# Kernel optimization log

Hardware: AMD Instinct MI355X
Metric: run time of the kernel (lower is better)

## Reference

```python
import jax, jax.numpy as jnp
import numpy as np

N_HEADS = 16
NEG_BIAS = -1000000000.0


def setup_inputs() -> dict:
    key = jax.random.key(0)
    k1, k2, k3, k4 = jax.random.split(key, 4)
    B, S, D = 2, 2048, 1024
    queries = jax.random.normal(k1, (B, S, D), dtype=jnp.float32)
    keys = jax.random.normal(k2, (B, S, D), dtype=jnp.float32)
    values = jax.random.normal(k3, (B, S, D), dtype=jnp.float32)
    mask = jax.random.randint(k4, (B, S, S), 0, 2, dtype=jnp.int32)
    return {"queries": queries, "keys": keys, "values": values, "mask": mask}


def _split_heads(x):
    B, S, D = x.shape
    return x.reshape(B, S, N_HEADS, D // N_HEADS).transpose(0, 2, 1, 3)  # [B,H,S,d]


def reference(queries, keys, values, mask):
    q = _split_heads(queries)   # [B,H,Sq,d]
    k = _split_heads(keys)      # [B,H,Sk,d]
    v = _split_heads(values)    # [B,H,Sk,d]
    d_head = q.shape[-1]
    # scaled dot product similarity
    sim = jnp.einsum('bhqd,bhkd->bhqk', q, k) / jnp.sqrt(jnp.float32(d_head))
    # additive mask (softmax attention function -> non-hadamard)
    bias = NEG_BIAS * (1.0 - mask.astype(sim.dtype))[:, None]  # [B,1,Sq,Sk]
    sim = sim + bias
    # softmax with max-subtraction (numerically stable, as in original)
    weights = jax.nn.softmax(sim, axis=-1)
    out = jnp.einsum('bhqk,bhkd->bhqd', weights, v)  # [B,H,Sq,d]
    B, H, Sq, d = out.shape
    return out.transpose(0, 2, 1, 3).reshape(B, Sq, H * d)
```

## Files before the change

### kernel.cpp

```cpp
#include <hip/hip_runtime.h>

#define S_LEN 2048
#define D_MODEL 1024
#define DH 64
#define BQ 64
#define BK 64
#define LDK 72
#define LDV 72
#define LDP 72
#define ZSCALE 0.18033688f
#define M0F    12.0f
#define ZBIAS  -1.5e9f

using short8 = __attribute__((ext_vector_type(8))) short;
using f32x4  = __attribute__((ext_vector_type(4))) float;
using uint2v = __attribute__((ext_vector_type(2))) unsigned int;

__device__ __forceinline__ unsigned short f2bf(float x) {
    union { float f; unsigned int u; } c; c.f = x;
    unsigned int u = c.u;
    u += 0x7fffu + ((u >> 16) & 1u);
    return (unsigned short)(u >> 16);
}

__global__ __launch_bounds__(256) void cvt_fused(const float* __restrict__ V,
                                                 const int* __restrict__ M,
                                                 const float* __restrict__ K,
                                                 unsigned short* __restrict__ VT,
                                                 unsigned long long* __restrict__ Mb,
                                                 unsigned short* __restrict__ KB) {
    const int blk = blockIdx.x;
    const int tid = threadIdx.x;
    if (blk < 1024) {
        __shared__ float tsF[64][65];
        const int b  = blk >> 9;
        const int h  = (blk >> 5) & 15;
        const int s0 = (blk & 31) * 64;
        #pragma unroll
        for (int it = 0; it < 2; ++it) {
            int seg = tid + it * 256;
            int s = seg >> 3, d8 = (seg & 7) << 3;
            const float* p = V + (size_t)(b * S_LEN + s0 + s) * D_MODEL + h * DH + d8;
            f32x4 a = *(const f32x4*)p;
            f32x4 c = *(const f32x4*)(p + 4);
            #pragma unroll
            for (int j = 0; j < 4; ++j) { tsF[s][d8 + j] = a[j]; tsF[s][d8 + 4 + j] = c[j]; }
        }
        __syncthreads();
        #pragma unroll
        for (int it = 0; it < 2; ++it) {
            int seg = tid + it * 256;
            int d = seg >> 3, s8 = (seg & 7) << 3;
            short8 w;
            #pragma unroll
            for (int j = 0; j < 8; ++j) w[j] = (short)f2bf(tsF[s8 + j][d]);
            *(short8*)(VT + ((size_t)((b * 16 + h) * 64 + d)) * S_LEN + s0 + s8) = w;
        }
    } else if (blk < 2048) {
        const int pb   = blk - 1024;
        const int wave = tid >> 6, lane = tid & 63;
        const int row  = pb * 4 + wave;
        const int* mp  = M + (size_t)row * S_LEN;
        #pragma unroll 4
        for (int it = 0; it < 32; ++it) {
            int m = mp[it * 64 + lane];
            unsigned long long bal = __ballot(m != 0);
            if (lane == 0) Mb[(size_t)row * 32 + it] = bal;
        }
    } else {
        size_t g = (size_t)(blk - 2048) * 256 + tid;
        size_t base = g * 16;
        f32x4 a0 = *(const f32x4*)(K + base);
        f32x4 a1 = *(const f32x4*)(K + base + 4);
        f32x4 a2 = *(const f32x4*)(K + base + 8);
        f32x4 a3 = *(const f32x4*)(K + base + 12);
        short8 w0, w1;
        #pragma unroll
        for (int j = 0; j < 4; ++j) {
            w0[j] = (short)f2bf(a0[j]); w0[4 + j] = (short)f2bf(a1[j]);
            w1[j] = (short)f2bf(a2[j]); w1[4 + j] = (short)f2bf(a3[j]);
        }
        *(short8*)(KB + base)     = w0;
        *(short8*)(KB + base + 8) = w1;
    }
}

__global__ __launch_bounds__(256) void mha_fwd_v3(
    const float* __restrict__ Q,
    const float* __restrict__ K,
    const unsigned short* __restrict__ KB,
    const unsigned short* __restrict__ VT,
    const unsigned int* __restrict__ Mw,
    float* __restrict__ O,
    int kbf)
{
    __shared__ alignas(16) unsigned short Ks[BK][LDK];
    __shared__ alignas(16) unsigned short Vt[DH][LDV];
    __shared__ alignas(16) unsigned short Ps[4][16][LDP];

    const int blk = blockIdx.x;
    const int b   = blk >> 9;
    const int h   = (blk >> 5) & 15;
    const int qbase = (blk & 31) * BQ;
    const int bh  = b * 16 + h;

    const int tid  = threadIdx.x;
    const int wave = tid >> 6;
    const int lane = tid & 63;
    const int n16  = lane & 15;
    const int quad = lane >> 4;

    const size_t qoff = (size_t)(b * S_LEN + qbase + wave * 16 + n16) * D_MODEL + h * DH + quad * 8;
    short8 qf0, qf1;
    {
        f32x4 a0 = *(const f32x4*)(Q + qoff);
        f32x4 a1 = *(const f32x4*)(Q + qoff + 4);
        f32x4 a2 = *(const f32x4*)(Q + qoff + 32);
        f32x4 a3 = *(const f32x4*)(Q + qoff + 36);
        #pragma unroll
        for (int j = 0; j < 4; ++j) {
            qf0[j] = (short)f2bf(a0[j]); qf0[4 + j] = (short)f2bf(a1[j]);
            qf1[j] = (short)f2bf(a2[j]); qf1[4 + j] = (short)f2bf(a3[j]);
        }
    }

    const short8 ones = {0x3F80,0x3F80,0x3F80,0x3F80,0x3F80,0x3F80,0x3F80,0x3F80};

    f32x4 o0 = {0.f,0.f,0.f,0.f}, o1 = o0, o2 = o0, o3 = o0, o4 = o0;

    size_t mwbase[4];
    #pragma unroll
    for (int r = 0; r < 4; ++r)
        mwbase[r] = ((size_t)(b * S_LEN + qbase + wave * 16 + quad * 4 + r)) * 64;

    for (int kb = 0; kb < S_LEN; kb += BK) {
        __syncthreads();
        if (kbf) {
            int seg = tid;
            #pragma unroll
            for (int it = 0; it < 2; ++it, seg += 256) {
                int row = seg >> 3, c8 = (seg & 7) << 3;
                *(short8*)&Ks[row][c8] =
                    *(const short8*)(KB + (size_t)(b * S_LEN + kb + row) * D_MODEL + h * DH + c8);
            }
        } else {
            int seg = tid;
            #pragma unroll
            for (int it = 0; it < 2; ++it, seg += 256) {
                int row = seg >> 3, c8 = (seg & 7) << 3;
                const float* kp = K + (size_t)(b * S_LEN + kb + row) * D_MODEL + h * DH + c8;
                f32x4 p0 = *(const f32x4*)kp;
                f32x4 p1 = *(const f32x4*)(kp + 4);
                short8 w;
                #pragma unroll
                for (int j = 0; j < 4; ++j) { w[j] = (short)f2bf(p0[j]); w[4 + j] = (short)f2bf(p1[j]); }
                *(short8*)&Ks[row][c8] = w;
            }
        }
        {
            int seg = tid;
            #pragma unroll
            for (int it = 0; it < 2; ++it, seg += 256) {
                int d = seg >> 3, k8 = (seg & 7) << 3;
                *(short8*)&Vt[d][k8] =
                    *(const short8*)(VT + ((size_t)(bh * 64 + d)) * S_LEN + kb + k8);
            }
        }
        __syncthreads();

        f32x4 s[4];
        #pragma unroll
        for (int ct = 0; ct < 4; ++ct) {
            short8 kf0 = *(const short8*)&Ks[ct * 16 + n16][     quad * 8];
            short8 kf1 = *(const short8*)&Ks[ct * 16 + n16][32 + quad * 8];
            f32x4 acc = {0.f,0.f,0.f,0.f};
            acc = __builtin_amdgcn_mfma_f32_16x16x32_bf16(qf0, kf0, acc, 0, 0, 0);
            acc = __builtin_amdgcn_mfma_f32_16x16x32_bf16(qf1, kf1, acc, 0, 0, 0);
            s[ct] = acc;
        }
        #pragma unroll
        for (int r = 0; r < 4; ++r) {
            uint2v mv = *(const uint2v*)(Mw + mwbase[r] + (kb >> 5));
            unsigned int b0 = mv[0] >> n16, b1 = mv[1] >> n16;
            s[0][r] = fmaf(s[0][r], ZSCALE, (b0 & 1u)         ? -M0F : ZBIAS);
            s[1][r] = fmaf(s[1][r], ZSCALE, ((b0 >> 16) & 1u) ? -M0F : ZBIAS);
            s[2][r] = fmaf(s[2][r], ZSCALE, (b1 & 1u)         ? -M0F : ZBIAS);
            s[3][r] = fmaf(s[3][r], ZSCALE, ((b1 >> 16) & 1u) ? -M0F : ZBIAS);
        }
        #pragma unroll
        for (int ct = 0; ct < 4; ++ct) {
            #pragma unroll
            for (int r = 0; r < 4; ++r) {
                float p = exp2f(s[ct][r]);
                Ps[wave][quad * 4 + r][ct * 16 + n16] =
                    (unsigned short)(__float_as_uint(p) >> 16);
            }
        }
        #pragma unroll
        for (int kc = 0; kc < 2; ++kc) {
            short8 af = *(const short8*)&Ps[wave][n16][kc * 32 + quad * 8];
            short8 v0 = *(const short8*)&Vt[      n16][kc * 32 + quad * 8];
            short8 v1 = *(const short8*)&Vt[16 + n16][kc * 32 + quad * 8];
            short8 v2 = *(const short8*)&Vt[32 + n16][kc * 32 + quad * 8];
            short8 v3 = *(const short8*)&Vt[48 + n16][kc * 32 + quad * 8];
            o0 = __builtin_amdgcn_mfma_f32_16x16x32_bf16(af, v0, o0, 0, 0, 0);
            o1 = __builtin_amdgcn_mfma_f32_16x16x32_bf16(af, v1, o1, 0, 0, 0);
            o2 = __builtin_amdgcn_mfma_f32_16x16x32_bf16(af, v2, o2, 0, 0, 0);
            o3 = __builtin_amdgcn_mfma_f32_16x16x32_bf16(af, v3, o3, 0, 0, 0);
            o4 = __builtin_amdgcn_mfma_f32_16x16x32_bf16(af, ones, o4, 0, 0, 0);
        }
    }

    #pragma unroll
    for (int r = 0; r < 4; ++r) {
        float rl = 1.f / o4[r];
        size_t row = (size_t)(b * S_LEN + qbase + wave * 16 + quad * 4 + r);
        float* op = O + row * D_MODEL + h * DH + n16;
        op[0]  = o0[r] * rl;
        op[16] = o1[r] * rl;
        op[32] = o2[r] * rl;
        op[48] = o3[r] * rl;
    }
}

extern "C" void kernel_launch(void* const* d_in, const int* in_sizes, int n_in,
                              void* d_out, int out_size, void* d_ws, size_t ws_size,
                              hipStream_t stream) {
    const float* Q = (const float*)d_in[0];
    const float* K = (const float*)d_in[1];
    const float* V = (const float*)d_in[2];
    const int*   M = (const int*)d_in[3];
    float*       O = (float*)d_out;

    const size_t NEL = (size_t)2 * S_LEN * D_MODEL;
    const size_t VT_BYTES = NEL * sizeof(unsigned short);
    const size_t KB_BYTES = NEL * sizeof(unsigned short);
    const size_t MB_BYTES = (size_t)2 * S_LEN * 32 * 8;

    if (ws_size >= VT_BYTES + KB_BYTES + MB_BYTES) {
        unsigned short* VT = (unsigned short*)d_ws;
        unsigned short* KB = (unsigned short*)((char*)d_ws + VT_BYTES);
        unsigned long long* Mb = (unsigned long long*)((char*)d_ws + VT_BYTES + KB_BYTES);
        hipLaunchKernelGGL(cvt_fused, dim3(3072), dim3(256), 0, stream, V, M, K, VT, Mb, KB);
        hipLaunchKernelGGL(mha_fwd_v3, dim3(1024), dim3(256), 0, stream,
                           Q, K, KB, VT, (const unsigned int*)Mb, O, 1);
    } else {
        unsigned short* VT = (unsigned short*)d_ws;
        unsigned long long* Mb = (unsigned long long*)((char*)d_ws + VT_BYTES);
        hipLaunchKernelGGL(cvt_fused, dim3(2048), dim3(256), 0, stream, V, M, K, VT, Mb, (unsigned short*)0);
        hipLaunchKernelGGL(mha_fwd_v3, dim3(1024), dim3(256), 0, stream,
                           Q, K, (const unsigned short*)0, VT, (const unsigned int*)Mb, O, 0);
    }
}
```

Before: 208.2 us.

## Prefetch next K/V tiles into registers and transpose score MFMA layout

```diff
diff --git a/kernel.cpp b/kernel.cpp
--- a/kernel.cpp
+++ b/kernel.cpp
@@ -13,8 +13,8 @@
 #define ZBIAS  -1.5e9f
 
 using short8 = __attribute__((ext_vector_type(8))) short;
+using s4v    = __attribute__((ext_vector_type(4))) short;
 using f32x4  = __attribute__((ext_vector_type(4))) float;
-using uint2v = __attribute__((ext_vector_type(2))) unsigned int;
 
 __device__ __forceinline__ unsigned short f2bf(float x) {
     union { float f; unsigned int u; } c; c.f = x;
@@ -68,29 +68,25 @@
             if (lane == 0) Mb[(size_t)row * 32 + it] = bal;
         }
     } else {
-        size_t g = (size_t)(blk - 2048) * 256 + tid;
-        size_t base = g * 16;
-        f32x4 a0 = *(const f32x4*)(K + base);
-        f32x4 a1 = *(const f32x4*)(K + base + 4);
-        f32x4 a2 = *(const f32x4*)(K + base + 8);
-        f32x4 a3 = *(const f32x4*)(K + base + 12);
-        short8 w0, w1;
-        #pragma unroll
-        for (int j = 0; j < 4; ++j) {
-            w0[j] = (short)f2bf(a0[j]); w0[4 + j] = (short)f2bf(a1[j]);
-            w1[j] = (short)f2bf(a2[j]); w1[4 + j] = (short)f2bf(a3[j]);
-        }
-        *(short8*)(KB + base)     = w0;
-        *(short8*)(KB + base + 8) = w1;
-    }
-}
-
-__global__ __launch_bounds__(256) void mha_fwd_v3(
+        size_t base = (size_t)(blk - 2048) * 4096;
+        #pragma unroll
+        for (int it = 0; it < 4; ++it) {
+            size_t i = base + ((size_t)(it * 256 + tid)) * 4;
+            f32x4 a = *(const f32x4*)(K + i);
+            s4v w;
+            #pragma unroll
+            for (int j = 0; j < 4; ++j) w[j] = (short)f2bf(a[j]);
+            *(s4v*)(KB + i) = w;
+        }
+    }
+}
+
+__global__ __launch_bounds__(256) void mha_fwd_v5(
     const float* __restrict__ Q,
     const float* __restrict__ K,
     const unsigned short* __restrict__ KB,
     const unsigned short* __restrict__ VT,
-    const unsigned int* __restrict__ Mw,
+    const unsigned long long* __restrict__ Mb,
     float* __restrict__ O,
     int kbf)
 {
@@ -109,6 +105,9 @@
     const int lane = tid & 63;
     const int n16  = lane & 15;
     const int quad = lane >> 4;
+    const int bsh  = quad << 2;
+
+    const int srow = tid >> 3, sc8 = (tid & 7) << 3;
 
     const size_t qoff = (size_t)(b * S_LEN + qbase + wave * 16 + n16) * D_MODEL + h * DH + quad * 8;
     short8 qf0, qf1;
@@ -128,74 +127,100 @@
 
     f32x4 o0 = {0.f,0.f,0.f,0.f}, o1 = o0, o2 = o0, o3 = o0, o4 = o0;
 
-    size_t mwbase[4];
-    #pragma unroll
-    for (int r = 0; r < 4; ++r)
-        mwbase[r] = ((size_t)(b * S_LEN + qbase + wave * 16 + quad * 4 + r)) * 64;
+    const unsigned long long* mrow = Mb + (size_t)(b * S_LEN + qbase + wave * 16 + n16) * 32;
+
+    const size_t kbase = (size_t)(b * S_LEN) * D_MODEL + h * DH;
+    const size_t vbase = (size_t)(bh * 64) * S_LEN;
+
+    short8 ka0, ka1, va0, va1;
+    if (kbf) {
+        ka0 = *(const short8*)(KB + kbase + (size_t)(srow)      * D_MODEL + sc8);
+        ka1 = *(const short8*)(KB + kbase + (size_t)(srow + 32) * D_MODEL + sc8);
+    } else {
+        const float* kp0 = K + kbase + (size_t)(srow)      * D_MODEL + sc8;
+        const float* kp1 = K + kbase + (size_t)(srow + 32) * D_MODEL + sc8;
+        f32x4 p0 = *(const f32x4*)kp0, p1 = *(const f32x4*)(kp0 + 4);
+        f32x4 p2 = *(const f32x4*)kp1, p3 = *(const f32x4*)(kp1 + 4);
+        #pragma unroll
+        for (int j = 0; j < 4; ++j) {
+            ka0[j] = (short)f2bf(p0[j]); ka0[4 + j] = (short)f2bf(p1[j]);
+            ka1[j] = (short)f2bf(p2[j]); ka1[4 + j] = (short)f2bf(p3[j]);
+        }
+    }
+    va0 = *(const short8*)(VT + vbase + (size_t)(srow)      * S_LEN + sc8);
+    va1 = *(const short8*)(VT + vbase + (size_t)(srow + 32) * S_LEN + sc8);
+    unsigned long long mw = mrow[0];
 
     for (int kb = 0; kb < S_LEN; kb += BK) {
         __syncthreads();
-        if (kbf) {
-            int seg = tid;
-            #pragma unroll
-            for (int it = 0; it < 2; ++it, seg += 256) {
-                int row = seg >> 3, c8 = (seg & 7) << 3;
-                *(short8*)&Ks[row][c8] =
-                    *(const short8*)(KB + (size_t)(b * S_LEN + kb + row) * D_MODEL + h * DH + c8);
+        *(short8*)&Ks[srow][sc8]      = ka0;
+        *(short8*)&Ks[srow + 32][sc8] = ka1;
+        *(short8*)&Vt[srow][sc8]      = va0;
+        *(short8*)&Vt[srow + 32][sc8] = va1;
+
+        const int kn = kb + BK;
+        const bool more = kn < S_LEN;
+        short8 nka0, nka1, nva0, nva1;
+        unsigned long long nmw;
+        if (more) {
+            if (kbf) {
+                nka0 = *(const short8*)(KB + kbase + (size_t)(kn + srow)      * D_MODEL + sc8);
+                nka1 = *(const short8*)(KB + kbase + (size_t)(kn + srow + 32) * D_MODEL + sc8);
+            } else {
+                const float* kp0 = K + kbase + (size_t)(kn + srow)      * D_MODEL + sc8;
+                const float* kp1 = K + kbase + (size_t)(kn + srow + 32) * D_MODEL + sc8;
+                f32x4 p0 = *(const f32x4*)kp0, p1 = *(const f32x4*)(kp0 + 4);
+                f32x4 p2 = *(const f32x4*)kp1, p3 = *(const f32x4*)(kp1 + 4);
+                #pragma unroll
+                for (int j = 0; j < 4; ++j) {
+                    nka0[j] = (short)f2bf(p0[j]); nka0[4 + j] = (short)f2bf(p1[j]);
+                    nka1[j] = (short)f2bf(p2[j]); nka1[4 + j] = (short)f2bf(p3[j]);
+                }
             }
-        } else {
-            int seg = tid;
-            #pragma unroll
-            for (int it = 0; it < 2; ++it, seg += 256) {
-                int row = seg >> 3, c8 = (seg & 7) << 3;
-                const float* kp = K + (size_t)(b * S_LEN + kb + row) * D_MODEL + h * DH + c8;
-                f32x4 p0 = *(const f32x4*)kp;
-                f32x4 p1 = *(const f32x4*)(kp + 4);
-                short8 w;
-                #pragma unroll
-                for (int j = 0; j < 4; ++j) { w[j] = (short)f2bf(p0[j]); w[4 + j] = (short)f2bf(p1[j]); }
-                *(short8*)&Ks[row][c8] = w;
-            }
-        }
-        {
-            int seg = tid;
-            #pragma unroll
-            for (int it = 0; it < 2; ++it, seg += 256) {
-                int d = seg >> 3, k8 = (seg & 7) << 3;
-                *(short8*)&Vt[d][k8] =
-                    *(const short8*)(VT + ((size_t)(bh * 64 + d)) * S_LEN + kb + k8);
-            }
+            nva0 = *(const short8*)(VT + vbase + (size_t)(srow)      * S_LEN + kn + sc8);
+            nva1 = *(const short8*)(VT + vbase + (size_t)(srow + 32) * S_LEN + kn + sc8);
+            nmw  = mrow[kn >> 6];
         }
         __syncthreads();
 
         f32x4 s[4];
+        __builtin_amdgcn_s_setprio(1);
         #pragma unroll
         for (int ct = 0; ct < 4; ++ct) {
             short8 kf0 = *(const short8*)&Ks[ct * 16 + n16][     quad * 8];
             short8 kf1 = *(const short8*)&Ks[ct * 16 + n16][32 + quad * 8];
             f32x4 acc = {0.f,0.f,0.f,0.f};
-            acc = __builtin_amdgcn_mfma_f32_16x16x32_bf16(qf0, kf0, acc, 0, 0, 0);
-            acc = __builtin_amdgcn_mfma_f32_16x16x32_bf16(qf1, kf1, acc, 0, 0, 0);
+            acc = __builtin_amdgcn_mfma_f32_16x16x32_bf16(kf0, qf0, acc, 0, 0, 0);
+            acc = __builtin_amdgcn_mfma_f32_16x16x32_bf16(kf1, qf1, acc, 0, 0, 0);
             s[ct] = acc;
         }
-        #pragma unroll
-        for (int r = 0; r < 4; ++r) {
-            uint2v mv = *(const uint2v*)(Mw + mwbase[r] + (kb >> 5));
-            unsigned int b0 = mv[0] >> n16, b1 = mv[1] >> n16;
-            s[0][r] = fmaf(s[0][r], ZSCALE, (b0 & 1u)         ? -M0F : ZBIAS);
-            s[1][r] = fmaf(s[1][r], ZSCALE, ((b0 >> 16) & 1u) ? -M0F : ZBIAS);
-            s[2][r] = fmaf(s[2][r], ZSCALE, (b1 & 1u)         ? -M0F : ZBIAS);
-            s[3][r] = fmaf(s[3][r], ZSCALE, ((b1 >> 16) & 1u) ? -M0F : ZBIAS);
+        __builtin_amdgcn_s_setprio(0);
+
+        {
+            unsigned int wlo = (unsigned int)mw;
+            unsigned int whi = (unsigned int)(mw >> 32);
+            #pragma unroll
+            for (int r = 0; r < 4; ++r) {
+                s[0][r] = fmaf(s[0][r], ZSCALE, ((wlo >> (bsh + r))      & 1u) ? -M0F : ZBIAS);
+                s[1][r] = fmaf(s[1][r], ZSCALE, ((wlo >> (bsh + r + 16)) & 1u) ? -M0F : ZBIAS);
+                s[2][r] = fmaf(s[2][r], ZSCALE, ((whi >> (bsh + r))      & 1u) ? -M0F : ZBIAS);
+                s[3][r] = fmaf(s[3][r], ZSCALE, ((whi >> (bsh + r + 16)) & 1u) ? -M0F : ZBIAS);
+            }
         }
         #pragma unroll
         for (int ct = 0; ct < 4; ++ct) {
-            #pragma unroll
-            for (int r = 0; r < 4; ++r) {
-                float p = exp2f(s[ct][r]);
-                Ps[wave][quad * 4 + r][ct * 16 + n16] =
-                    (unsigned short)(__float_as_uint(p) >> 16);
-            }
-        }
+            unsigned int p0 = __float_as_uint(exp2f(s[ct][0]));
+            unsigned int p1 = __float_as_uint(exp2f(s[ct][1]));
+            unsigned int p2 = __float_as_uint(exp2f(s[ct][2]));
+            unsigned int p3 = __float_as_uint(exp2f(s[ct][3]));
+            s4v dv;
+            dv[0] = (short)(p0 >> 16);
+            dv[1] = (short)(p1 >> 16);
+            dv[2] = (short)(p2 >> 16);
+            dv[3] = (short)(p3 >> 16);
+            *(s4v*)&Ps[wave][n16][ct * 16 + bsh] = dv;
+        }
+        __builtin_amdgcn_s_setprio(1);
         #pragma unroll
         for (int kc = 0; kc < 2; ++kc) {
             short8 af = *(const short8*)&Ps[wave][n16][kc * 32 + quad * 8];
@@ -209,6 +234,9 @@
             o3 = __builtin_amdgcn_mfma_f32_16x16x32_bf16(af, v3, o3, 0, 0, 0);
             o4 = __builtin_amdgcn_mfma_f32_16x16x32_bf16(af, ones, o4, 0, 0, 0);
         }
+        __builtin_amdgcn_s_setprio(0);
+
+        if (more) { ka0 = nka0; ka1 = nka1; va0 = nva0; va1 = nva1; mw = nmw; }
     }
 
     #pragma unroll
@@ -242,13 +270,13 @@
         unsigned short* KB = (unsigned short*)((char*)d_ws + VT_BYTES);
         unsigned long long* Mb = (unsigned long long*)((char*)d_ws + VT_BYTES + KB_BYTES);
         hipLaunchKernelGGL(cvt_fused, dim3(3072), dim3(256), 0, stream, V, M, K, VT, Mb, KB);
-        hipLaunchKernelGGL(mha_fwd_v3, dim3(1024), dim3(256), 0, stream,
-                           Q, K, KB, VT, (const unsigned int*)Mb, O, 1);
+        hipLaunchKernelGGL(mha_fwd_v5, dim3(1024), dim3(256), 0, stream,
+                           Q, K, KB, VT, Mb, O, 1);
     } else {
         unsigned short* VT = (unsigned short*)d_ws;
         unsigned long long* Mb = (unsigned long long*)((char*)d_ws + VT_BYTES);
         hipLaunchKernelGGL(cvt_fused, dim3(2048), dim3(256), 0, stream, V, M, K, VT, Mb, (unsigned short*)0);
-        hipLaunchKernelGGL(mha_fwd_v3, dim3(1024), dim3(256), 0, stream,
-                           Q, K, (const unsigned short*)0, VT, (const unsigned int*)Mb, O, 0);
-    }
-}
+        hipLaunchKernelGGL(mha_fwd_v5, dim3(1024), dim3(256), 0, stream,
+                           Q, K, (const unsigned short*)0, VT, Mb, O, 0);
+    }
+}
```

Measured after the change: 195.0 us. 1.07x faster.
